# Optimization experiments

Measured on AMD Instinct MI355X. Metric: run time of the kernel, lower is better.

## Reference

```python
import jax, jax.numpy as jnp
import numpy as np

N = 50000
E = 800000


def gcn_conv(h_in, W, b, src, dst, n_nodes):
    # h_in: [N, Fin] -> linear transform first (PyG GCNConv default)
    h = h_in @ W  # [N, Fout]
    # add self loops
    loop = jnp.arange(n_nodes, dtype=src.dtype)
    s = jnp.concatenate([src, loop])
    d = jnp.concatenate([dst, loop])
    # symmetric normalization: deg computed on destination with unit edge weights
    deg = jax.ops.segment_sum(jnp.ones_like(s, dtype=h.dtype), d, num_segments=n_nodes)
    dinv = jnp.where(deg > 0, jax.lax.rsqrt(deg), 0.0)
    norm = dinv[s] * dinv[d]  # [E+N]
    # gather source features, scale, scatter-add to destinations
    msg = h[s] * norm[:, None]  # [E+N, Fout]
    out = jax.ops.segment_sum(msg, d, num_segments=n_nodes)
    return out + b


def setup_inputs() -> dict:
    key = jax.random.key(0)
    ks = jax.random.split(key, 6)
    x = jax.random.normal(ks[0], (N, 256), dtype=jnp.float32)
    edge_index = jax.random.randint(ks[1], (2, E), 0, N, dtype=jnp.int64)
    # Glorot-style scaling for weights
    W1 = jax.random.normal(ks[2], (256, 128), dtype=jnp.float32) * (1.0 / np.sqrt(256))
    b1 = jnp.zeros((128,), dtype=jnp.float32)
    W2 = jax.random.normal(ks[3], (128, 64), dtype=jnp.float32) * (1.0 / np.sqrt(128))
    b2 = jnp.zeros((64,), dtype=jnp.float32)
    return {"x": x, "edge_index": edge_index, "W1": W1, "b1": b1, "W2": W2, "b2": b2}


def reference(x, edge_index, W1, b1, W2, b2):
    src, dst = edge_index[0], edge_index[1]
    h = gcn_conv(x, W1, b1, src, dst, N)
    h = jax.nn.relu(h)
    out = gcn_conv(h, W2, b2, src, dst, N)
    return out
```

## Files before the change

### kernel.cpp

```cpp
#include <hip/hip_runtime.h>

#define FIN   256
#define F1    128
#define F2    64

typedef _Float16 f16x8 __attribute__((ext_vector_type(8)));
typedef _Float16 f16x4 __attribute__((ext_vector_type(4)));
typedef float    f32x4 __attribute__((ext_vector_type(4)));

#define BUCKET_SHIFT 7
#define BUCKET_W     128
#define MAXBUCK      512
#define CAP          2560
#define CHUNK        2048

__global__ __launch_bounds__(256) void prep(const float* __restrict__ W1,
                                            const float* __restrict__ W2,
                                            _Float16* __restrict__ WT1,
                                            _Float16* __restrict__ WT2,
                                            int* __restrict__ bcur_pad) {
    int b = blockIdx.x;
    if (b == 0) {
        for (int i = threadIdx.x; i < MAXBUCK; i += 256) bcur_pad[i * 16] = i * CAP;
        return;
    }
    int idx = (b - 1) * 256 + threadIdx.x;
    if (idx < FIN * F1) {
        int k = idx / F1, n = idx % F1;
        WT1[(size_t)n * FIN + k] = (_Float16)W1[idx];
    } else {
        int j = idx - FIN * F1;
        if (j < F1 * F2) {
            int k = j / F2, n = j % F2;
            WT2[(size_t)n * F1 + k] = (_Float16)W2[j];
        }
    }
}

__global__ __launch_bounds__(512) void bucket_fill(const int* __restrict__ src,
                                                   const int* __restrict__ dst,
                                                   int* __restrict__ bcur_pad,
                                                   unsigned* __restrict__ ebuf, int E) {
    __shared__ int h[MAXBUCK];
    __shared__ int base[MAXBUCK];
    for (int i = threadIdx.x; i < MAXBUCK; i += 512) h[i] = 0;
    __syncthreads();
    int cbase = blockIdx.x * CHUNK;
    int lim   = min(cbase + CHUNK, E);
    for (int e = cbase + threadIdx.x; e < lim; e += 512)
        atomicAdd(&h[dst[e] >> BUCKET_SHIFT], 1);
    __syncthreads();
    for (int i = threadIdx.x; i < MAXBUCK; i += 512) {
        int c = h[i];
        base[i] = c ? atomicAdd(&bcur_pad[i * 16], c) : 0;
        h[i] = 0;
    }
    __syncthreads();
    for (int e = cbase + threadIdx.x; e < lim; e += 512) {
        int d = dst[e], b = d >> BUCKET_SHIFT;
        int r = atomicAdd(&h[b], 1);
        int pos = base[b] + r;
        if (pos < (b + 1) * CAP)
            ebuf[pos] = ((unsigned)src[e] << BUCKET_SHIFT) | (unsigned)(d & (BUCKET_W - 1));
    }
}

__global__ __launch_bounds__(512) void csr_build(const unsigned* __restrict__ ebuf,
                                                 const int* __restrict__ bcur_pad,
                                                 unsigned* __restrict__ rowinfo,
                                                 float* __restrict__ dinv,
                                                 int* __restrict__ csr, int n) {
    __shared__ int cnt[BUCKET_W];
    __shared__ int sbuf[2][BUCKET_W];
    __shared__ int lcur[BUCKET_W];
    int k = blockIdx.x, t = threadIdx.x;
    int ebeg = k * CAP;
    int cntk = min(bcur_pad[k * 16] - ebeg, CAP);
    if (t < BUCKET_W) cnt[t] = 0;
    __syncthreads();
    for (int e = t; e < cntk; e += 512)
        atomicAdd(&cnt[ebuf[ebeg + e] & (BUCKET_W - 1)], 1);
    __syncthreads();
    int myc = (t < BUCKET_W) ? cnt[t] : 0;
    if (t < BUCKET_W) sbuf[0][t] = myc;
    __syncthreads();
    int cur = 0;
    for (int off = 1; off < BUCKET_W; off <<= 1) {
        if (t < BUCKET_W) {
            int v = sbuf[cur][t];
            if (t >= off) v += sbuf[cur][t - off];
            sbuf[cur ^ 1][t] = v;
        }
        cur ^= 1;
        __syncthreads();
    }
    if (t < BUCKET_W) {
        int excl = sbuf[cur][t] - myc;
        int beg  = ebeg + excl;
        lcur[t] = beg;
        int node = (k << BUCKET_SHIFT) + t;
        if (node < n) {
            rowinfo[node] = ((unsigned)beg << 8) | (unsigned)min(myc, 255);
            dinv[node]    = rsqrtf((float)(myc + 1));
        }
    }
    __syncthreads();
    for (int e = t; e < cntk; e += 512) {
        unsigned ed = ebuf[ebeg + e];
        int pos = atomicAdd(&lcur[ed & (BUCKET_W - 1)], 1);
        csr[pos] = (int)(ed >> BUCKET_SHIFT);
    }
}

template <int BN, int K, typename AT>
__global__ __launch_bounds__(256) void gemm_mfma(const AT* __restrict__ A,
                                                 const _Float16* __restrict__ WT,
                                                 const float* __restrict__ dinv,
                                                 _Float16* __restrict__ Ch, int M) {
    constexpr int NB = BN / 16;
    constexpr int CH = K / 32;
    constexpr int KP = K + 8;
    __shared__ _Float16 Bs[BN][KP];

    int tid  = threadIdx.x;
    int wave = tid >> 6, lane = tid & 63;
    int col  = lane & 15, kg = lane >> 4;
    int row0 = blockIdx.x * 64;
    int arow = row0 + wave * 16 + col;
    bool rowok = arow < M;

    float4 paf[sizeof(AT) == 4 ? 2 * CH : 1];
    f16x8  pah[sizeof(AT) == 2 ? CH : 1];
    const AT* Ab = A + (size_t)arow * K + kg * 8;
    if constexpr (sizeof(AT) == 4) {
#pragma unroll
        for (int c = 0; c < CH; ++c) {
            paf[2 * c]     = make_float4(0.f, 0.f, 0.f, 0.f);
            paf[2 * c + 1] = make_float4(0.f, 0.f, 0.f, 0.f);
            if (rowok) {
                paf[2 * c]     = *(const float4*)((const float*)Ab + c * 32);
                paf[2 * c + 1] = *(const float4*)((const float*)Ab + c * 32 + 4);
            }
        }
    } else {
#pragma unroll
        for (int c = 0; c < CH; ++c) {
            pah[c] = (f16x8){0, 0, 0, 0, 0, 0, 0, 0};
            if (rowok) pah[c] = *(const f16x8*)((const _Float16*)Ab + c * 32);
        }
    }

    constexpr int TOT = BN * K / 8;
#pragma unroll
    for (int l = 0; l < TOT / 256; ++l) {
        int u  = l * 256 + tid;
        int r  = u / (K / 8);
        int c8 = u % (K / 8);
        *(f16x8*)&Bs[r][c8 * 8] = *(const f16x8*)&WT[(size_t)r * K + c8 * 8];
    }
    __syncthreads();

    f32x4 acc[NB];
#pragma unroll
    for (int j = 0; j < NB; ++j) acc[j] = (f32x4){0.f, 0.f, 0.f, 0.f};

#pragma unroll
    for (int c = 0; c < CH; ++c) {
        f16x8 a;
        if constexpr (sizeof(AT) == 4) {
            float4 lo = paf[2 * c], hi = paf[2 * c + 1];
            a[0] = (_Float16)lo.x; a[1] = (_Float16)lo.y;
            a[2] = (_Float16)lo.z; a[3] = (_Float16)lo.w;
            a[4] = (_Float16)hi.x; a[5] = (_Float16)hi.y;
            a[6] = (_Float16)hi.z; a[7] = (_Float16)hi.w;
        } else {
            a = pah[c];
        }
#pragma unroll
        for (int j = 0; j < NB; ++j) {
            f16x8 b = *(const f16x8*)&Bs[j * 16 + col][c * 32 + kg * 8];
            acc[j] = __builtin_amdgcn_mfma_f32_16x16x32_f16(a, b, acc[j], 0, 0, 0);
        }
    }

    int rbase = row0 + wave * 16 + kg * 4;
#pragma unroll
    for (int r = 0; r < 4; ++r) {
        int m = rbase + r;
        if (m < M) {
            float dv = dinv[m];
#pragma unroll
            for (int j = 0; j < NB; ++j)
                Ch[(size_t)m * BN + j * 16 + col] = (_Float16)(dv * acc[j][r]);
        }
    }
}

__global__ __launch_bounds__(256) void agg1_gemm2(const _Float16* __restrict__ Hs,
                                                  const unsigned* __restrict__ rowinfo,
                                                  const int* __restrict__ csr,
                                                  const float* __restrict__ dinv,
                                                  const float* __restrict__ bias,
                                                  const _Float16* __restrict__ WT2,
                                                  _Float16* __restrict__ Hs2, int n) {
    constexpr int KP = F1 + 8;
    __shared__ _Float16 Xs[64][KP];
    __shared__ _Float16 Ws[F2][KP];

    int tid = threadIdx.x;

    f16x8 wreg[4];
#pragma unroll
    for (int l = 0; l < 4; ++l)
        wreg[l] = *(const f16x8*)&WT2[(l * 256 + tid) * 8];

    int node0 = blockIdx.x * 64;
    int sub = tid & 15;
    int grp = tid >> 4;
    const int col = sub * 8;

#pragma unroll
    for (int r = 0; r < 4; ++r) {
        int nloc = r * 16 + grp;
        int gid  = node0 + nloc;
        f16x8 t = (f16x8){0, 0, 0, 0, 0, 0, 0, 0};
        if (gid < n) {
            float a[8];
            {
                f16x8 h = *(const f16x8*)&Hs[(size_t)gid * F1 + col];
#pragma unroll
                for (int i = 0; i < 8; ++i) a[i] = (float)h[i];
            }
            unsigned ri = rowinfo[gid];
            int e   = (int)(ri >> 8);
            int end = e + (int)(ri & 255u);
            for (; e + 8 <= end; e += 8) {
                int s0 = csr[e + 0], s1 = csr[e + 1], s2 = csr[e + 2], s3 = csr[e + 3];
                int s4 = csr[e + 4], s5 = csr[e + 5], s6 = csr[e + 6], s7 = csr[e + 7];
                f16x8 v0 = *(const f16x8*)&Hs[(size_t)s0 * F1 + col];
                f16x8 v1 = *(const f16x8*)&Hs[(size_t)s1 * F1 + col];
                f16x8 v2 = *(const f16x8*)&Hs[(size_t)s2 * F1 + col];
                f16x8 v3 = *(const f16x8*)&Hs[(size_t)s3 * F1 + col];
                f16x8 v4 = *(const f16x8*)&Hs[(size_t)s4 * F1 + col];
                f16x8 v5 = *(const f16x8*)&Hs[(size_t)s5 * F1 + col];
                f16x8 v6 = *(const f16x8*)&Hs[(size_t)s6 * F1 + col];
                f16x8 v7 = *(const f16x8*)&Hs[(size_t)s7 * F1 + col];
#pragma unroll
                for (int i = 0; i < 8; ++i)
                    a[i] += (((float)v0[i] + (float)v1[i]) + ((float)v2[i] + (float)v3[i]))
                          + (((float)v4[i] + (float)v5[i]) + ((float)v6[i] + (float)v7[i]));
            }
            for (; e + 4 <= end; e += 4) {
                int s0 = csr[e + 0], s1 = csr[e + 1], s2 = csr[e + 2], s3 = csr[e + 3];
                f16x8 v0 = *(const f16x8*)&Hs[(size_t)s0 * F1 + col];
                f16x8 v1 = *(const f16x8*)&Hs[(size_t)s1 * F1 + col];
                f16x8 v2 = *(const f16x8*)&Hs[(size_t)s2 * F1 + col];
                f16x8 v3 = *(const f16x8*)&Hs[(size_t)s3 * F1 + col];
#pragma unroll
                for (int i = 0; i < 8; ++i)
                    a[i] += ((float)v0[i] + (float)v1[i]) + ((float)v2[i] + (float)v3[i]);
            }
            for (; e < end; ++e) {
                int s = csr[e];
                f16x8 v = *(const f16x8*)&Hs[(size_t)s * F1 + col];
#pragma unroll
                for (int i = 0; i < 8; ++i) a[i] += (float)v[i];
            }
            float dv = dinv[gid];
            float4 bb0 = *(const float4*)&bias[col];
            float4 bb1 = *(const float4*)&bias[col + 4];
            float o[8];
            o[0] = dv * a[0] + bb0.x; o[1] = dv * a[1] + bb0.y;
            o[2] = dv * a[2] + bb0.z; o[3] = dv * a[3] + bb0.w;
            o[4] = dv * a[4] + bb1.x; o[5] = dv * a[5] + bb1.y;
            o[6] = dv * a[6] + bb1.z; o[7] = dv * a[7] + bb1.w;
#pragma unroll
            for (int i = 0; i < 8; ++i) t[i] = (_Float16)fmaxf(o[i], 0.f);
        }
        *(f16x8*)&Xs[nloc][col] = t;
    }

#pragma unroll
    for (int l = 0; l < 4; ++l) {
        int u  = l * 256 + tid;
        int rr = u >> 4, c8 = u & 15;
        *(f16x8*)&Ws[rr][c8 * 8] = wreg[l];
    }
    __syncthreads();

    int wave = tid >> 6, lane = tid & 63;
    int mcol = lane & 15, kg = lane >> 4;
    f32x4 acc[4];
#pragma unroll
    for (int j = 0; j < 4; ++j) acc[j] = (f32x4){0.f, 0.f, 0.f, 0.f};
#pragma unroll
    for (int c = 0; c < 4; ++c) {
        f16x8 a = *(const f16x8*)&Xs[wave * 16 + mcol][c * 32 + kg * 8];
#pragma unroll
        for (int j = 0; j < 4; ++j) {
            f16x8 b = *(const f16x8*)&Ws[j * 16 + mcol][c * 32 + kg * 8];
            acc[j] = __builtin_amdgcn_mfma_f32_16x16x32_f16(a, b, acc[j], 0, 0, 0);
        }
    }
    int rbase = node0 + wave * 16 + kg * 4;
#pragma unroll
    for (int r = 0; r < 4; ++r) {
        int m = rbase + r;
        if (m < n) {
            float dv = dinv[m];
#pragma unroll
            for (int j = 0; j < 4; ++j)
                Hs2[(size_t)m * F2 + j * 16 + mcol] = (_Float16)(dv * acc[j][r]);
        }
    }
}

template <int F, bool RELU, typename OutT>
__global__ __launch_bounds__(256) void aggregate(const _Float16* __restrict__ Hs,
                                                 const unsigned* __restrict__ rowinfo,
                                                 const int* __restrict__ csr,
                                                 const float* __restrict__ dinv,
                                                 const float* __restrict__ bias,
                                                 OutT* __restrict__ out, int n) {
    constexpr int LPG = F / 8;
    int gid = (blockIdx.x * blockDim.x + threadIdx.x) / LPG;
    int sub = threadIdx.x & (LPG - 1);
    if (gid >= n) return;
    const int col = sub * 8;

    float a[8];
    {
        f16x8 h = *(const f16x8*)&Hs[(size_t)gid * F + col];
#pragma unroll
        for (int i = 0; i < 8; ++i) a[i] = (float)h[i];
    }

    unsigned ri = rowinfo[gid];
    int e   = (int)(ri >> 8);
    int end = e + (int)(ri & 255u);

    for (; e + 8 <= end; e += 8) {
        int s0 = csr[e + 0], s1 = csr[e + 1], s2 = csr[e + 2], s3 = csr[e + 3];
        int s4 = csr[e + 4], s5 = csr[e + 5], s6 = csr[e + 6], s7 = csr[e + 7];
        f16x8 v0 = *(const f16x8*)&Hs[(size_t)s0 * F + col];
        f16x8 v1 = *(const f16x8*)&Hs[(size_t)s1 * F + col];
        f16x8 v2 = *(const f16x8*)&Hs[(size_t)s2 * F + col];
        f16x8 v3 = *(const f16x8*)&Hs[(size_t)s3 * F + col];
        f16x8 v4 = *(const f16x8*)&Hs[(size_t)s4 * F + col];
        f16x8 v5 = *(const f16x8*)&Hs[(size_t)s5 * F + col];
        f16x8 v6 = *(const f16x8*)&Hs[(size_t)s6 * F + col];
        f16x8 v7 = *(const f16x8*)&Hs[(size_t)s7 * F + col];
#pragma unroll
        for (int i = 0; i < 8; ++i) {
            a[i] += (((float)v0[i] + (float)v1[i]) + ((float)v2[i] + (float)v3[i]))
                  + (((float)v4[i] + (float)v5[i]) + ((float)v6[i] + (float)v7[i]));
        }
    }
    for (; e + 4 <= end; e += 4) {
        int s0 = csr[e + 0], s1 = csr[e + 1], s2 = csr[e + 2], s3 = csr[e + 3];
        f16x8 v0 = *(const f16x8*)&Hs[(size_t)s0 * F + col];
        f16x8 v1 = *(const f16x8*)&Hs[(size_t)s1 * F + col];
        f16x8 v2 = *(const f16x8*)&Hs[(size_t)s2 * F + col];
        f16x8 v3 = *(const f16x8*)&Hs[(size_t)s3 * F + col];
#pragma unroll
        for (int i = 0; i < 8; ++i)
            a[i] += ((float)v0[i] + (float)v1[i]) + ((float)v2[i] + (float)v3[i]);
    }
    for (; e < end; ++e) {
        int s = csr[e];
        f16x8 v = *(const f16x8*)&Hs[(size_t)s * F + col];
#pragma unroll
        for (int i = 0; i < 8; ++i) a[i] += (float)v[i];
    }

    float dv = dinv[gid];
    float4 bb0 = *(const float4*)&bias[col];
    float4 bb1 = *(const float4*)&bias[col + 4];
    float o[8];
    o[0] = dv * a[0] + bb0.x; o[1] = dv * a[1] + bb0.y;
    o[2] = dv * a[2] + bb0.z; o[3] = dv * a[3] + bb0.w;
    o[4] = dv * a[4] + bb1.x; o[5] = dv * a[5] + bb1.y;
    o[6] = dv * a[6] + bb1.z; o[7] = dv * a[7] + bb1.w;
    if (RELU) {
#pragma unroll
        for (int i = 0; i < 8; ++i) o[i] = fmaxf(o[i], 0.f);
    }
    if constexpr (sizeof(OutT) == 2) {
        f16x8 ov;
#pragma unroll
        for (int i = 0; i < 8; ++i) ov[i] = (_Float16)o[i];
        *(f16x8*)&out[(size_t)gid * F + col] = ov;
    } else {
        float4 ov0 = make_float4(o[0], o[1], o[2], o[3]);
        float4 ov1 = make_float4(o[4], o[5], o[6], o[7]);
        *(float4*)&out[(size_t)gid * F + col]     = ov0;
        *(float4*)&out[(size_t)gid * F + col + 4] = ov1;
    }
}

extern "C" void kernel_launch(void* const* d_in, const int* in_sizes, int n_in,
                              void* d_out, int out_size, void* d_ws, size_t ws_size,
                              hipStream_t stream) {
    const float* x  = (const float*)d_in[0];
    const int*   ei = (const int*)d_in[1];
    const float* W1 = (const float*)d_in[2];
    const float* b1 = (const float*)d_in[3];
    const float* W2 = (const float*)d_in[4];
    const float* b2 = (const float*)d_in[5];
    float* out = (float*)d_out;

    const int N = in_sizes[0] / FIN;
    const int E = in_sizes[1] / 2;
    const int* src = ei;
    const int* dst = ei + E;

    char* w = (char*)d_ws;
    auto alloc = [&](size_t bytes) {
        void* p = (void*)w;
        w += (bytes + 255) & ~(size_t)255;
        return p;
    };
    float*    dinv     = (float*)alloc((size_t)N * 4);
    unsigned* rowinfo  = (unsigned*)alloc((size_t)N * 4);
    int*      csr      = (int*)alloc((size_t)MAXBUCK * CAP * 4);
    int*      bcur_pad = (int*)alloc((size_t)MAXBUCK * 16 * 4);
    unsigned* ebuf     = (unsigned*)alloc((size_t)MAXBUCK * CAP * 4);
    _Float16* WT1      = (_Float16*)alloc((size_t)FIN * F1 * 2);
    _Float16* WT2      = (_Float16*)alloc((size_t)F1 * F2 * 2);
    _Float16* Hs1      = (_Float16*)alloc((size_t)N * F1 * 2);
    _Float16* Hs2      = (_Float16*)alloc((size_t)N * F2 * 2);

    const int nbuck  = (N + BUCKET_W - 1) >> BUCKET_SHIFT;
    const int nchunk = (E + CHUNK - 1) / CHUNK;
    const int nprep  = 1 + (FIN * F1 + F1 * F2 + 255) / 256;

    prep<<<nprep, 256, 0, stream>>>(W1, W2, WT1, WT2, bcur_pad);
    bucket_fill<<<nchunk, 512, 0, stream>>>(src, dst, bcur_pad, ebuf, E);
    csr_build<<<nbuck, 512, 0, stream>>>(ebuf, bcur_pad, rowinfo, dinv, csr, N);

    gemm_mfma<F1, FIN, float><<<(N + 63) / 64, 256, 0, stream>>>(x, WT1, dinv, Hs1, N);

    agg1_gemm2<<<(N + 63) / 64, 256, 0, stream>>>(Hs1, rowinfo, csr, dinv, b1, WT2, Hs2, N);

    {
        int blocks = (int)(((size_t)N * (F2 / 8) + 255) / 256);
        aggregate<F2, false, float><<<blocks, 256, 0, stream>>>(Hs2, rowinfo, csr, dinv, b2, out, N);
    }
}
```

Measured before the change: 105.2 us.

## Pad CSR rows to multiples of eight with a zero sentinel row

Each CSR row is padded to a multiple of eight entries. The pad slots point to an extra zeroed feature row at index N, so both aggregation kernels run only the 8-wide unrolled gather loop with no 4-wide or scalar remainder loops. The bucket and CSR build kernels also keep their edges in registers instead of re-reading global memory between the count and scatter passes. The cost is extra gathers of the zero row, plus a larger CSR buffer and an extra feature row in the workspace.

```diff
diff --git a/kernel.cpp b/kernel.cpp
--- a/kernel.cpp
+++ b/kernel.cpp
@@ -12,27 +12,33 @@
 #define BUCKET_W     128
 #define MAXBUCK      512
 #define CAP          2560
+#define CSRCAP       3584
 #define CHUNK        2048
 
 __global__ __launch_bounds__(256) void prep(const float* __restrict__ W1,
                                             const float* __restrict__ W2,
                                             _Float16* __restrict__ WT1,
                                             _Float16* __restrict__ WT2,
-                                            int* __restrict__ bcur_pad) {
+                                            int* __restrict__ bcur_pad,
+                                            _Float16* __restrict__ Hs1,
+                                            _Float16* __restrict__ Hs2, int n) {
     int b = blockIdx.x;
+    int t = threadIdx.x;
     if (b == 0) {
-        for (int i = threadIdx.x; i < MAXBUCK; i += 256) bcur_pad[i * 16] = i * CAP;
+        for (int i = t; i < MAXBUCK; i += 256) bcur_pad[i * 16] = i * CAP;
+        if (t < F1) Hs1[(size_t)n * F1 + t] = (_Float16)0.f;
+        if (t < F2) Hs2[(size_t)n * F2 + t] = (_Float16)0.f;
         return;
     }
-    int idx = (b - 1) * 256 + threadIdx.x;
+    int idx = (b - 1) * 256 + t;
     if (idx < FIN * F1) {
-        int k = idx / F1, n = idx % F1;
-        WT1[(size_t)n * FIN + k] = (_Float16)W1[idx];
+        int k = idx / F1, nn = idx % F1;
+        WT1[(size_t)nn * FIN + k] = (_Float16)W1[idx];
     } else {
         int j = idx - FIN * F1;
         if (j < F1 * F2) {
-            int k = j / F2, n = j % F2;
-            WT2[(size_t)n * F1 + k] = (_Float16)W2[j];
+            int k = j / F2, nn = j % F2;
+            WT2[(size_t)nn * F1 + k] = (_Float16)W2[j];
         }
     }
 }
@@ -47,8 +53,14 @@
     __syncthreads();
     int cbase = blockIdx.x * CHUNK;
     int lim   = min(cbase + CHUNK, E);
-    for (int e = cbase + threadIdx.x; e < lim; e += 512)
-        atomicAdd(&h[dst[e] >> BUCKET_SHIFT], 1);
+    int sd[CHUNK / 512], dd[CHUNK / 512];
+    int ne = 0;
+    for (int e = cbase + threadIdx.x; e < lim; e += 512) {
+        sd[ne] = src[e];
+        dd[ne] = dst[e];
+        ++ne;
+    }
+    for (int i = 0; i < ne; ++i) atomicAdd(&h[dd[i] >> BUCKET_SHIFT], 1);
     __syncthreads();
     for (int i = threadIdx.x; i < MAXBUCK; i += 512) {
         int c = h[i];
@@ -56,12 +68,12 @@
         h[i] = 0;
     }
     __syncthreads();
-    for (int e = cbase + threadIdx.x; e < lim; e += 512) {
-        int d = dst[e], b = d >> BUCKET_SHIFT;
+    for (int i = 0; i < ne; ++i) {
+        int d = dd[i], b = d >> BUCKET_SHIFT;
         int r = atomicAdd(&h[b], 1);
         int pos = base[b] + r;
         if (pos < (b + 1) * CAP)
-            ebuf[pos] = ((unsigned)src[e] << BUCKET_SHIFT) | (unsigned)(d & (BUCKET_W - 1));
+            ebuf[pos] = ((unsigned)sd[i] << BUCKET_SHIFT) | (unsigned)(d & (BUCKET_W - 1));
     }
 }
 
@@ -76,13 +88,16 @@
     int k = blockIdx.x, t = threadIdx.x;
     int ebeg = k * CAP;
     int cntk = min(bcur_pad[k * 16] - ebeg, CAP);
+    unsigned ed[(CAP + 511) / 512];
+    int ne = 0;
+    for (int e = t; e < cntk; e += 512) ed[ne++] = ebuf[ebeg + e];
     if (t < BUCKET_W) cnt[t] = 0;
     __syncthreads();
-    for (int e = t; e < cntk; e += 512)
-        atomicAdd(&cnt[ebuf[ebeg + e] & (BUCKET_W - 1)], 1);
+    for (int i = 0; i < ne; ++i) atomicAdd(&cnt[ed[i] & (BUCKET_W - 1)], 1);
     __syncthreads();
     int myc = (t < BUCKET_W) ? cnt[t] : 0;
-    if (t < BUCKET_W) sbuf[0][t] = myc;
+    int pc  = (myc + 7) & ~7;
+    if (t < BUCKET_W) sbuf[0][t] = pc;
     __syncthreads();
     int cur = 0;
     for (int off = 1; off < BUCKET_W; off <<= 1) {
@@ -94,9 +109,10 @@
         cur ^= 1;
         __syncthreads();
     }
+    int beg = 0;
     if (t < BUCKET_W) {
-        int excl = sbuf[cur][t] - myc;
-        int beg  = ebeg + excl;
+        int excl = sbuf[cur][t] - pc;
+        beg = k * CSRCAP + excl;
         lcur[t] = beg;
         int node = (k << BUCKET_SHIFT) + t;
         if (node < n) {
@@ -105,10 +121,13 @@
         }
     }
     __syncthreads();
-    for (int e = t; e < cntk; e += 512) {
-        unsigned ed = ebuf[ebeg + e];
-        int pos = atomicAdd(&lcur[ed & (BUCKET_W - 1)], 1);
-        csr[pos] = (int)(ed >> BUCKET_SHIFT);
+    for (int i = 0; i < ne; ++i) {
+        int pos = atomicAdd(&lcur[ed[i] & (BUCKET_W - 1)], 1);
+        csr[pos] = (int)(ed[i] >> BUCKET_SHIFT);
+    }
+    __syncthreads();
+    if (t < BUCKET_W) {
+        for (int p = beg + myc; p < beg + pc; ++p) csr[p] = n;
     }
 }
 
@@ -233,8 +252,8 @@
             }
             unsigned ri = rowinfo[gid];
             int e   = (int)(ri >> 8);
-            int end = e + (int)(ri & 255u);
-            for (; e + 8 <= end; e += 8) {
+            int end = e + (((int)(ri & 255u) + 7) & ~7);
+            for (; e < end; e += 8) {
                 int s0 = csr[e + 0], s1 = csr[e + 1], s2 = csr[e + 2], s3 = csr[e + 3];
                 int s4 = csr[e + 4], s5 = csr[e + 5], s6 = csr[e + 6], s7 = csr[e + 7];
                 f16x8 v0 = *(const f16x8*)&Hs[(size_t)s0 * F1 + col];
@@ -249,22 +268,6 @@
                 for (int i = 0; i < 8; ++i)
                     a[i] += (((float)v0[i] + (float)v1[i]) + ((float)v2[i] + (float)v3[i]))
                           + (((float)v4[i] + (float)v5[i]) + ((float)v6[i] + (float)v7[i]));
-            }
-            for (; e + 4 <= end; e += 4) {
-                int s0 = csr[e + 0], s1 = csr[e + 1], s2 = csr[e + 2], s3 = csr[e + 3];
-                f16x8 v0 = *(const f16x8*)&Hs[(size_t)s0 * F1 + col];
-                f16x8 v1 = *(const f16x8*)&Hs[(size_t)s1 * F1 + col];
-                f16x8 v2 = *(const f16x8*)&Hs[(size_t)s2 * F1 + col];
-                f16x8 v3 = *(const f16x8*)&Hs[(size_t)s3 * F1 + col];
-#pragma unroll
-                for (int i = 0; i < 8; ++i)
-                    a[i] += ((float)v0[i] + (float)v1[i]) + ((float)v2[i] + (float)v3[i]);
-            }
-            for (; e < end; ++e) {
-                int s = csr[e];
-                f16x8 v = *(const f16x8*)&Hs[(size_t)s * F1 + col];
-#pragma unroll
-                for (int i = 0; i < 8; ++i) a[i] += (float)v[i];
             }
             float dv = dinv[gid];
             float4 bb0 = *(const float4*)&bias[col];
@@ -337,9 +340,9 @@
 
     unsigned ri = rowinfo[gid];
     int e   = (int)(ri >> 8);
-    int end = e + (int)(ri & 255u);
-
-    for (; e + 8 <= end; e += 8) {
+    int end = e + (((int)(ri & 255u) + 7) & ~7);
+
+    for (; e < end; e += 8) {
         int s0 = csr[e + 0], s1 = csr[e + 1], s2 = csr[e + 2], s3 = csr[e + 3];
         int s4 = csr[e + 4], s5 = csr[e + 5], s6 = csr[e + 6], s7 = csr[e + 7];
         f16x8 v0 = *(const f16x8*)&Hs[(size_t)s0 * F + col];
@@ -356,22 +359,6 @@
                   + (((float)v4[i] + (float)v5[i]) + ((float)v6[i] + (float)v7[i]));
         }
     }
-    for (; e + 4 <= end; e += 4) {
-        int s0 = csr[e + 0], s1 = csr[e + 1], s2 = csr[e + 2], s3 = csr[e + 3];
-        f16x8 v0 = *(const f16x8*)&Hs[(size_t)s0 * F + col];
-        f16x8 v1 = *(const f16x8*)&Hs[(size_t)s1 * F + col];
-        f16x8 v2 = *(const f16x8*)&Hs[(size_t)s2 * F + col];
-        f16x8 v3 = *(const f16x8*)&Hs[(size_t)s3 * F + col];
-#pragma unroll
-        for (int i = 0; i < 8; ++i)
-            a[i] += ((float)v0[i] + (float)v1[i]) + ((float)v2[i] + (float)v3[i]);
-    }
-    for (; e < end; ++e) {
-        int s = csr[e];
-        f16x8 v = *(const f16x8*)&Hs[(size_t)s * F + col];
-#pragma unroll
-        for (int i = 0; i < 8; ++i) a[i] += (float)v[i];
-    }
 
     float dv = dinv[gid];
     float4 bb0 = *(const float4*)&bias[col];
@@ -422,19 +409,19 @@
     };
     float*    dinv     = (float*)alloc((size_t)N * 4);
     unsigned* rowinfo  = (unsigned*)alloc((size_t)N * 4);
-    int*      csr      = (int*)alloc((size_t)MAXBUCK * CAP * 4);
+    int*      csr      = (int*)alloc((size_t)MAXBUCK * CSRCAP * 4);
     int*      bcur_pad = (int*)alloc((size_t)MAXBUCK * 16 * 4);
     unsigned* ebuf     = (unsigned*)alloc((size_t)MAXBUCK * CAP * 4);
     _Float16* WT1      = (_Float16*)alloc((size_t)FIN * F1 * 2);
     _Float16* WT2      = (_Float16*)alloc((size_t)F1 * F2 * 2);
-    _Float16* Hs1      = (_Float16*)alloc((size_t)N * F1 * 2);
-    _Float16* Hs2      = (_Float16*)alloc((size_t)N * F2 * 2);
+    _Float16* Hs1      = (_Float16*)alloc((size_t)(N + 1) * F1 * 2);
+    _Float16* Hs2      = (_Float16*)alloc((size_t)(N + 1) * F2 * 2);
 
     const int nbuck  = (N + BUCKET_W - 1) >> BUCKET_SHIFT;
     const int nchunk = (E + CHUNK - 1) / CHUNK;
     const int nprep  = 1 + (FIN * F1 + F1 * F2 + 255) / 256;
 
-    prep<<<nprep, 256, 0, stream>>>(W1, W2, WT1, WT2, bcur_pad);
+    prep<<<nprep, 256, 0, stream>>>(W1, W2, WT1, WT2, bcur_pad, Hs1, Hs2, N);
     bucket_fill<<<nchunk, 512, 0, stream>>>(src, dst, bcur_pad, ebuf, E);
     csr_build<<<nbuck, 512, 0, stream>>>(ebuf, bcur_pad, rowinfo, dinv, csr, N);
 
```

Result: faster. 101.4 us (-3.6%).
